# Optimization experiments

Hardware: AMD Instinct MI355X
Metric: run time of the kernel (lower is better)

The kernel has to match this reference:

```python
import jax, jax.numpy as jnp
import numpy as np

B, N, NB = 16, 768, 6144   # structures, atoms, bonds
L = 20.0                   # cubic cell edge (Angstrom)
BOTOL = 0.001              # bond-order cutoff ('cutoff' ffield param)
BO1_SI, BO2_SI, R0_SI = -0.077, 6.0, 1.39
BO1_PI, BO2_PI, R0_PI = -0.150, 5.0, 1.30
BO1_PP, BO2_PP, R0_PP = -0.300, 4.0, 1.25


def taper(r, rmin=0.001, rmax=0.002):
    # faithful translation of the torch taper(): smooth 0->1 switch on (rmin, rmax]
    r3 = jnp.where(r > rmax, 1.0, 0.0)
    ok = (r <= rmax) & (r > rmin)
    r2 = jnp.where(ok, r, 0.0)
    r20 = jnp.where(ok, 1.0, 0.0)
    rterm = 1.0 / (rmin - rmax) ** 3
    rm = rmin * r20
    rd = rm - r2
    trm1 = rm + 2.0 * r2 - 3.0 * rmax * r20
    return rterm * rd * rd * trm1 + r3


def tiny_mlp(X, wi, bi_, w, b, wo, bo_):
    # fmessage/fnn: sigmoid(matmul+bias) input layer, `layer` hidden layers, output layer
    h = jax.nn.sigmoid(X @ wi + bi_)          # [B,E,hid]
    for l in range(w.shape[0]):               # fixed small layer count (5)
        h = jax.nn.sigmoid(h @ w[l] + b[l])
    return jax.nn.sigmoid(h @ wo + bo_)


def _bop(r_, bo1, bo2, r0):
    # uncorrected bond-order term with taper near the cutoff (I-ReaxFF style)
    eterm = (1.0 + BOTOL) * jnp.exp(bo1 * (r_ / r0) ** bo2)
    return taper(eterm, BOTOL, 2.0 * BOTOL) * (eterm - BOTOL)


def _energy(x, cell, rcell, bi, bj, fm_wi, fm_bi, fm_w, fm_b, fm_wo, fm_bo,
            fe_wi, fe_bi, fe_w, fe_b, fe_wo, fe_bo, desi):
    # fvr: vr[b,i,j] = x[b,i] - x[b,j]  -> [B,N,N,3]
    vr = x[:, :, None, :] - x[:, None, :, :]
    vrf = jnp.einsum('bijk,bkl->bijl', vr, rcell)
    vrf = jnp.where(vrf - 0.5 > 0, vrf - 1.0, vrf)   # minimum image
    vrf = jnp.where(vrf + 0.5 < 0, vrf + 1.0, vrf)
    vr = jnp.einsum('bijk,bkl->bijl', vrf, cell)
    r = jnp.sqrt(jnp.sum(vr * vr, axis=3) + 1e-8)    # [B,N,N]
    rbd = r[:, bi, bj]                               # gather bonds -> [B,E]
    bop_si = _bop(rbd, BO1_SI, BO2_SI, R0_SI)
    bop_pi = _bop(rbd, BO1_PI, BO2_PI, R0_PI)
    bop_pp = _bop(rbd, BO1_PP, BO2_PP, R0_PP)
    feats = jnp.stack([bop_si, bop_pi, bop_pp], axis=2)        # [B,E,3]
    bo = tiny_mlp(feats, fm_wi, fm_bi, fm_w, fm_b, fm_wo, fm_bo)  # fmessage -> (bosi,bopi,bopp) [B,E,3]
    esi = tiny_mlp(bo, fe_wi, fe_bi, fe_w, fe_b, fe_wo, fe_bo)[..., 0]  # fnn 'fe' -> [B,E]
    ebd = -desi * esi                                # -Desi * esi per bond
    return jnp.sum(ebd, axis=1)                      # ebond per structure [B]


def setup_inputs() -> dict:
    key = jax.random.key(0)
    ks = jax.random.split(key, 16)
    s = 0.5
    x = jax.random.uniform(ks[0], (B, N, 3), jnp.float32) * L
    cell = jnp.tile(L * jnp.eye(3, dtype=jnp.float32), (B, 1, 1))
    rcell = jnp.tile(jnp.eye(3, dtype=jnp.float32) / L, (B, 1, 1))
    bdid = jax.random.randint(ks[1], (NB, 2), 0, N, dtype=jnp.int32)
    return {
        'x': x, 'cell': cell, 'rcell': rcell,
        'fm_wi': jax.random.normal(ks[2], (3, 9), jnp.float32) * s,
        'fm_bi': jax.random.normal(ks[3], (9,), jnp.float32) * s,
        'fm_w': jax.random.normal(ks[4], (5, 9, 9), jnp.float32) * s,
        'fm_b': jax.random.normal(ks[5], (5, 9), jnp.float32) * s,
        'fm_wo': jax.random.normal(ks[6], (9, 3), jnp.float32) * s,
        'fm_bo': jax.random.normal(ks[7], (3,), jnp.float32) * s,
        'fe_wi': jax.random.normal(ks[8], (3, 8), jnp.float32) * s,
        'fe_bi': jax.random.normal(ks[9], (8,), jnp.float32) * s,
        'fe_w': jax.random.normal(ks[10], (5, 8, 8), jnp.float32) * s,
        'fe_b': jax.random.normal(ks[11], (5, 8), jnp.float32) * s,
        'fe_wo': jax.random.normal(ks[12], (8, 1), jnp.float32) * s,
        'fe_bo': jax.random.normal(ks[13], (1,), jnp.float32) * s,
        'desi': jnp.float32(120.0),
        'bdid': bdid,
    }


def reference(x, cell, rcell, fm_wi, fm_bi, fm_w, fm_b, fm_wo, fm_bo,
              fe_wi, fe_bi, fe_w, fe_b, fe_wo, fe_bo, desi, bdid):
    bi, bj = bdid[:, 0], bdid[:, 1]
    params = (fm_wi, fm_bi, fm_w, fm_b, fm_wo, fm_bo,
              fe_wi, fe_bi, fe_w, fe_b, fe_wo, fe_bo, desi)
    E = _energy(x, cell, rcell, bi, bj, *params)               # [B]
    # get_forces: force = -dE/dx (autograd), as in the torch module
    force = -jax.grad(lambda xx: jnp.sum(_energy(xx, cell, rcell, bi, bj, *params)))(x)
    return (E, force)
```

## Files before the change

### kernel.cpp

```cpp
#include <hip/hip_runtime.h>

#define BB 16
#define NN 768
#define NBOND 6144
#define BOTOLF 0.001f

#define THREADS        128
#define BLKS_PER_BATCH 48
#define BONDS_PER_BLK  128
#define NPART          (BB * BLKS_PER_BATCH)
#define FELEMS         (NN * 3)

typedef float f32x2 __attribute__((ext_vector_type(2)));

#define L_FM_WI 0
#define L_FM_BI 36
#define L_FM_W  48
#define L_FM_B  588
#define L_FM_WO 648
#define L_FM_BO 684
#define L_FE_WI 688
#define L_FE_BI 712
#define L_FE_W  720
#define L_FE_B  1040
#define L_FE_WO 1080
#define L_FE_BO 1088
#define WTOT    1092

__device__ __forceinline__ float frcp(float x)  { return __builtin_amdgcn_rcpf(x); }
__device__ __forceinline__ float frsq(float x)  { return __builtin_amdgcn_rsqf(x); }

__device__ __forceinline__ float sigf(float z) {
    return frcp(1.0f + __expf(-z));
}

__device__ __forceinline__ f32x2 sig2(f32x2 z) {
    float s = sigf(z.x);
    f32x2 r;
    r.x = s;
    r.y = s * (1.0f - s) * z.y;
    return r;
}

__device__ __forceinline__ f32x2 bop_calc(float r, float inv_r, float bo1, float r0i, int ibo2)
{
    float t = r * r0i;
    float t2 = t * t;
    float p;
    if (ibo2 == 6)      p = t2 * t2 * t2;
    else if (ibo2 == 5) p = t2 * t2 * t;
    else                p = t2 * t2;
    float e = (1.0f + BOTOLF) * __expf(bo1 * p);
    float de_dr = e * bo1 * (float)ibo2 * p * inv_r;

    const float rmin = BOTOLF, rmax = 2.0f * BOTOLF;
    float T, dT;
    if (e > rmax) { T = 1.0f; dT = 0.0f; }
    else if (e > rmin) {
        const float rterm = -1.0e9f;
        float rd   = rmin - e;
        float trm1 = rmin + 2.0f * e - 3.0f * rmax;
        T  = rterm * rd * rd * trm1;
        dT = rterm * 2.0f * rd * (rd - trm1);
    } else { T = 0.0f; dT = 0.0f; }

    f32x2 out;
    out.x = T * (e - BOTOLF);
    out.y = (dT * (e - BOTOLF) + T) * de_dr;
    return out;
}

template<int NIN, int NOUT, int PAD>
__device__ __forceinline__ void dense1(const float* __restrict__ wb, const float* __restrict__ bb,
                                       const f32x2* __restrict__ h, f32x2* __restrict__ o)
{
    f32x2 z[NOUT];
    #pragma unroll
    for (int j = 0; j < NOUT; j++) { z[j].x = bb[j]; z[j].y = 0.0f; }
    #pragma unroll
    for (int k = 0; k < NIN; k++) {
        const float* row = wb + k * PAD;
        #pragma unroll
        for (int j = 0; j < NOUT; j++) z[j] += h[k] * row[j];
    }
    #pragma unroll
    for (int j = 0; j < NOUT; j++) o[j] = sig2(z[j]);
}

__global__ __launch_bounds__(THREADS) void reaxff_bond_kernel(
    const float* __restrict__ x, const float* __restrict__ cell, const float* __restrict__ rcell,
    const float* __restrict__ fm_wi, const float* __restrict__ fm_bi,
    const float* __restrict__ fm_w,  const float* __restrict__ fm_b,
    const float* __restrict__ fm_wo, const float* __restrict__ fm_bo,
    const float* __restrict__ fe_wi, const float* __restrict__ fe_bi,
    const float* __restrict__ fe_w,  const float* __restrict__ fe_b,
    const float* __restrict__ fe_wo, const float* __restrict__ fe_bo,
    const float* __restrict__ desi_p, const int* __restrict__ bdid,
    float* __restrict__ fpart,
    float* __restrict__ epart)
{
    __shared__ alignas(16) float w[WTOT];
    __shared__ alignas(16) float fsh[FELEMS];
    __shared__ float esum[2];
    const int tid = threadIdx.x;

    const int b = blockIdx.x / BLKS_PER_BATCH;
    const int k = (blockIdx.x % BLKS_PER_BATCH) * BONDS_PER_BLK + tid;

    const int2 bij = ((const int2*)bdid)[k];
    const int ai = bij.x, aj = bij.y;
    const float* xi = x + (size_t)(b * NN + ai) * 3;
    const float* xj = x + (size_t)(b * NN + aj) * 3;
    float xi0 = xi[0], xi1 = xi[1], xi2 = xi[2];
    float xj0 = xj[0], xj1 = xj[1], xj2 = xj[2];

    #pragma unroll 1
    for (int i = tid; i < FELEMS; i += THREADS) fsh[i] = 0.0f;

    #pragma unroll 1
    for (int idx = tid; idx < 36; idx += THREADS) {
        int r = idx / 12, c = idx % 12;
        w[L_FM_WI + idx] = (c < 9) ? fm_wi[r * 9 + c] : 0.0f;
    }
    #pragma unroll 1
    for (int idx = tid; idx < 12; idx += THREADS)
        w[L_FM_BI + idx] = (idx < 9) ? fm_bi[idx] : 0.0f;
    #pragma unroll 1
    for (int idx = tid; idx < 540; idx += THREADS) {
        int l = idx / 108, rem = idx % 108, r = rem / 12, c = rem % 12;
        w[L_FM_W + idx] = (c < 9) ? fm_w[l * 81 + r * 9 + c] : 0.0f;
    }
    #pragma unroll 1
    for (int idx = tid; idx < 60; idx += THREADS) {
        int l = idx / 12, c = idx % 12;
        w[L_FM_B + idx] = (c < 9) ? fm_b[l * 9 + c] : 0.0f;
    }
    #pragma unroll 1
    for (int idx = tid; idx < 36; idx += THREADS) {
        int r = idx / 4, c = idx % 4;
        w[L_FM_WO + idx] = (c < 3) ? fm_wo[r * 3 + c] : 0.0f;
    }
    if (tid < 4)  w[L_FM_BO + tid] = (tid < 3) ? fm_bo[tid] : 0.0f;
    if (tid < 24) w[L_FE_WI + tid] = fe_wi[tid];
    if (tid < 8)  w[L_FE_BI + tid] = fe_bi[tid];
    #pragma unroll 1
    for (int idx = tid; idx < 320; idx += THREADS) w[L_FE_W + idx] = fe_w[idx];
    if (tid < 40) w[L_FE_B + tid]  = fe_b[tid];
    if (tid < 8)  w[L_FE_WO + tid] = fe_wo[tid];
    if (tid == 0) { w[L_FE_BO] = fe_bo[0]; w[L_FE_BO+1]=0; w[L_FE_BO+2]=0; w[L_FE_BO+3]=0; }
    __syncthreads();

    const float* cb = cell  + b * 9;
    const float* rb = rcell + b * 9;
    const float D  = desi_p[0];

    float u0 = xi0 - xj0;
    float u1 = xi1 - xj1;
    float u2 = xi2 - xj2;

    float f0 = u0 * rb[0] + u1 * rb[3] + u2 * rb[6];
    float f1 = u0 * rb[1] + u1 * rb[4] + u2 * rb[7];
    float f2 = u0 * rb[2] + u1 * rb[5] + u2 * rb[8];
    f0 = (f0 - 0.5f > 0.0f) ? f0 - 1.0f : f0;  f0 = (f0 + 0.5f < 0.0f) ? f0 + 1.0f : f0;
    f1 = (f1 - 0.5f > 0.0f) ? f1 - 1.0f : f1;  f1 = (f1 + 0.5f < 0.0f) ? f1 + 1.0f : f1;
    f2 = (f2 - 0.5f > 0.0f) ? f2 - 1.0f : f2;  f2 = (f2 + 0.5f < 0.0f) ? f2 + 1.0f : f2;
    float v0 = f0 * cb[0] + f1 * cb[3] + f2 * cb[6];
    float v1 = f0 * cb[1] + f1 * cb[4] + f2 * cb[7];
    float v2 = f0 * cb[2] + f1 * cb[5] + f2 * cb[8];

    float r2sum = v0 * v0 + v1 * v1 + v2 * v2 + 1e-8f;
    float inv_r = frsq(r2sum);
    float r     = r2sum * inv_r;

    float cv0 = cb[0] * v0 + cb[1] * v1 + cb[2] * v2;
    float cv1 = cb[3] * v0 + cb[4] * v1 + cb[5] * v2;
    float cv2 = cb[6] * v0 + cb[7] * v1 + cb[8] * v2;
    float mv0 = rb[0] * cv0 + rb[1] * cv1 + rb[2] * cv2;
    float mv1 = rb[3] * cv0 + rb[4] * cv1 + rb[5] * cv2;
    float mv2 = rb[6] * cv0 + rb[7] * cv1 + rb[8] * cv2;

    f32x2 h[9], t[9];
    h[0] = bop_calc(r, inv_r, -0.077f, 1.0f / 1.39f, 6);
    h[1] = bop_calc(r, inv_r, -0.15f,  1.0f / 1.30f, 5);
    h[2] = bop_calc(r, inv_r, -0.30f,  1.0f / 1.25f, 4);

    dense1<3, 9, 12>(w + L_FM_WI, w + L_FM_BI, h, t);
    #pragma unroll
    for (int j = 0; j < 9; j++) h[j] = t[j];
    #pragma unroll 1
    for (int l = 0; l < 5; l++) {
        dense1<9, 9, 12>(w + L_FM_W + l * 108, w + L_FM_B + l * 12, h, t);
        #pragma unroll
        for (int j = 0; j < 9; j++) h[j] = t[j];
    }
    f32x2 bo3[3];
    dense1<9, 3, 4>(w + L_FM_WO, w + L_FM_BO, h, bo3);

    f32x2 g[8], s[8];
    dense1<3, 8, 8>(w + L_FE_WI, w + L_FE_BI, bo3, g);
    #pragma unroll 1
    for (int l = 0; l < 5; l++) {
        dense1<8, 8, 8>(w + L_FE_W + l * 64, w + L_FE_B + l * 8, g, s);
        #pragma unroll
        for (int j = 0; j < 8; j++) g[j] = s[j];
    }
    f32x2 z; z.x = w[L_FE_BO]; z.y = 0.0f;
    #pragma unroll
    for (int kk = 0; kk < 8; kk++) z += g[kk] * w[L_FE_WO + kk];
    f32x2 esi = sig2(z);

    float ebd = -D * esi.x;
    float gg  = -D * esi.y;
    float G0 = gg * mv0 * inv_r;
    float G1 = gg * mv1 * inv_r;
    float G2 = gg * mv2 * inv_r;
    atomicAdd(&fsh[ai * 3 + 0], -G0);
    atomicAdd(&fsh[ai * 3 + 1], -G1);
    atomicAdd(&fsh[ai * 3 + 2], -G2);
    atomicAdd(&fsh[aj * 3 + 0],  G0);
    atomicAdd(&fsh[aj * 3 + 1],  G1);
    atomicAdd(&fsh[aj * 3 + 2],  G2);

    float e = ebd;
    #pragma unroll
    for (int off = 32; off > 0; off >>= 1) e += __shfl_down(e, off, 64);
    if ((tid & 63) == 0) esum[tid >> 6] = e;

    __syncthreads();

    float4* dst = (float4*)(fpart + (size_t)blockIdx.x * FELEMS);
    const float4* src = (const float4*)fsh;
    #pragma unroll 1
    for (int i = tid; i < FELEMS / 4; i += THREADS)
        dst[i] = src[i];
    if (tid == 0) epart[blockIdx.x] = esum[0] + esum[1];
}

__global__ __launch_bounds__(256) void reaxff_reduce_kernel(
    const float* __restrict__ fpart, const float* __restrict__ epart,
    float* __restrict__ out)
{
    const int blk = blockIdx.x;
    const int tid = threadIdx.x;

    if (blk < (BB * FELEMS) / 256) {
        const int o = blk * 256 + tid;
        const int b = o / FELEMS;
        const int i = o - b * FELEMS;
        const float* base = fpart + ((size_t)b * BLKS_PER_BATCH) * FELEMS + i;
        float acc = 0.0f;
        #pragma unroll
        for (int p = 0; p < BLKS_PER_BATCH; p++)
            acc += base[(size_t)p * FELEMS];
        out[BB + o] = acc;
    } else {
        if (tid < BB) {
            const float* base = epart + tid * BLKS_PER_BATCH;
            float acc = 0.0f;
            #pragma unroll
            for (int p = 0; p < BLKS_PER_BATCH; p++)
                acc += base[p];
            out[tid] = acc;
        }
    }
}

extern "C" void kernel_launch(void* const* d_in, const int* in_sizes, int n_in,
                              void* d_out, int out_size, void* d_ws, size_t ws_size,
                              hipStream_t stream)
{
    float* fpart = (float*)d_ws;
    float* epart = fpart + (size_t)NPART * FELEMS;

    reaxff_bond_kernel<<<dim3(NPART), dim3(THREADS), 0, stream>>>(
        (const float*)d_in[0],  (const float*)d_in[1],  (const float*)d_in[2],
        (const float*)d_in[3],  (const float*)d_in[4],  (const float*)d_in[5],
        (const float*)d_in[6],  (const float*)d_in[7],  (const float*)d_in[8],
        (const float*)d_in[9],  (const float*)d_in[10], (const float*)d_in[11],
        (const float*)d_in[12], (const float*)d_in[13], (const float*)d_in[14],
        (const float*)d_in[15], (const int*)d_in[16],
        fpart, epart);

    reaxff_reduce_kernel<<<dim3((BB * FELEMS) / 256 + 1), dim3(256), 0, stream>>>(
        fpart, epart, (float*)d_out);
}
```

Baseline: 26.72 us.

## Fuse force reduction into bond kernel via last-block atomic counter

Removes the separate reduction kernel. Each block increments a per-structure counter after writing its partial forces and energy, and the last block for a structure sums all partials into the output. This is meant to remove a kernel launch and the gap between the two stages. In exchange the final reduction is confined to 16 blocks, and a memset of the counters is added before the launch.

New measurement: 92.18 us. 3.45x slower.

```diff
diff --git a/kernel.cpp b/kernel.cpp
--- a/kernel.cpp
+++ b/kernel.cpp
@@ -97,11 +97,14 @@
     const float* __restrict__ fe_wo, const float* __restrict__ fe_bo,
     const float* __restrict__ desi_p, const int* __restrict__ bdid,
     float* __restrict__ fpart,
-    float* __restrict__ epart)
+    float* __restrict__ epart,
+    unsigned* __restrict__ ctr,
+    float* __restrict__ out)
 {
     __shared__ alignas(16) float w[WTOT];
     __shared__ alignas(16) float fsh[FELEMS];
     __shared__ float esum[2];
+    __shared__ unsigned lastflag;
     const int tid = threadIdx.x;
 
     const int b = blockIdx.x / BLKS_PER_BATCH;
@@ -234,33 +237,35 @@
     for (int i = tid; i < FELEMS / 4; i += THREADS)
         dst[i] = src[i];
     if (tid == 0) epart[blockIdx.x] = esum[0] + esum[1];
-}
-
-__global__ __launch_bounds__(256) void reaxff_reduce_kernel(
-    const float* __restrict__ fpart, const float* __restrict__ epart,
-    float* __restrict__ out)
-{
-    const int blk = blockIdx.x;
-    const int tid = threadIdx.x;
-
-    if (blk < (BB * FELEMS) / 256) {
-        const int o = blk * 256 + tid;
-        const int b = o / FELEMS;
-        const int i = o - b * FELEMS;
-        const float* base = fpart + ((size_t)b * BLKS_PER_BATCH) * FELEMS + i;
-        float acc = 0.0f;
-        #pragma unroll
-        for (int p = 0; p < BLKS_PER_BATCH; p++)
-            acc += base[(size_t)p * FELEMS];
-        out[BB + o] = acc;
-    } else {
-        if (tid < BB) {
-            const float* base = epart + tid * BLKS_PER_BATCH;
-            float acc = 0.0f;
+
+    __threadfence();
+    __syncthreads();
+    if (tid == 0) {
+        unsigned old = atomicAdd(&ctr[b], 1u);
+        lastflag = (old == BLKS_PER_BATCH - 1) ? 1u : 0u;
+    }
+    __syncthreads();
+
+    if (lastflag) {
+        __threadfence();
+        const float4* fp4 = (const float4*)(fpart + (size_t)b * BLKS_PER_BATCH * FELEMS);
+        float4* o4 = (float4*)(out + BB + (size_t)b * FELEMS);
+        #pragma unroll 1
+        for (int idx = tid; idx < FELEMS / 4; idx += THREADS) {
+            float4 acc = {0.0f, 0.0f, 0.0f, 0.0f};
+            #pragma unroll 16
+            for (int p = 0; p < BLKS_PER_BATCH; p++) {
+                float4 v = fp4[(size_t)p * (FELEMS / 4) + idx];
+                acc.x += v.x; acc.y += v.y; acc.z += v.z; acc.w += v.w;
+            }
+            o4[idx] = acc;
+        }
+        if (tid == 0) {
+            float es = 0.0f;
             #pragma unroll
             for (int p = 0; p < BLKS_PER_BATCH; p++)
-                acc += base[p];
-            out[tid] = acc;
+                es += epart[b * BLKS_PER_BATCH + p];
+            out[b] = es;
         }
     }
 }
@@ -271,6 +276,9 @@
 {
     float* fpart = (float*)d_ws;
     float* epart = fpart + (size_t)NPART * FELEMS;
+    unsigned* ctr = (unsigned*)(epart + NPART);
+
+    hipMemsetAsync(ctr, 0, BB * sizeof(unsigned), stream);
 
     reaxff_bond_kernel<<<dim3(NPART), dim3(THREADS), 0, stream>>>(
         (const float*)d_in[0],  (const float*)d_in[1],  (const float*)d_in[2],
@@ -279,8 +287,5 @@
         (const float*)d_in[9],  (const float*)d_in[10], (const float*)d_in[11],
         (const float*)d_in[12], (const float*)d_in[13], (const float*)d_in[14],
         (const float*)d_in[15], (const int*)d_in[16],
-        fpart, epart);
-
-    reaxff_reduce_kernel<<<dim3((BB * FELEMS) / 256 + 1), dim3(256), 0, stream>>>(
-        fpart, epart, (float*)d_out);
-}
+        fpart, epart, ctr, (float*)d_out);
+}
```
